# Performance work log

Hardware: AMD Instinct MI355X
Metric: run time of the kernel (lower is better)

Reference implementation:

```python
import jax, jax.numpy as jnp
import numpy as np

H = 2048  # hidden_size
B = 16    # batch
S = 2048  # source (values) length
T = 16    # decoder state length per layer
L = 1     # num_layers


def setup_inputs() -> dict:
    key = jax.random.key(0)
    ks = jax.random.split(key, 6)
    sc = 1.0 / np.sqrt(H)
    return {
        "query": jax.random.normal(ks[0], (L, B, T, H), dtype=jnp.float32),
        "values": jax.random.normal(ks[1], (B, S, H), dtype=jnp.float32),
        "mask": jnp.ones((B, S), dtype=jnp.bool_),  # unused by the module
        "W1_w": jax.random.normal(ks[2], (H, H), dtype=jnp.float32) * sc,
        "W1_b": jnp.zeros((H,), dtype=jnp.float32),
        "W2_w": jax.random.normal(ks[3], (H, H), dtype=jnp.float32) * sc,
        "W2_b": jnp.zeros((H,), dtype=jnp.float32),
        "V_w": jax.random.normal(ks[4], (H,), dtype=jnp.float32) * sc,
        "V_b": jnp.zeros((), dtype=jnp.float32),
    }


def reference(query, values, mask, W1_w, W1_b, W2_w, W2_b, V_w, V_b):
    # query: (L,B,T,H); non-bidirectional path keeps last time step of layer 0
    q = query[0][:, -1:, :]                        # (B,1,H)
    q_proj = q @ W1_w.T + W1_b                     # (B,1,H)
    # Faithful quirk of the source: W2 is applied to values[0] (batch elem 0)
    v_proj = values[0] @ W2_w.T + W2_b             # (S,H)
    # broadcast add -> (B,S,H), tanh, project with V -> (B,S)
    scores = jnp.tanh(q_proj + v_proj[None, :, :]) @ V_w + V_b  # (B,S)
    scores = scores[:, None, :]                    # (B,1,S)
    alphas = jax.nn.softmax(scores, axis=-1)       # (B,1,S)
    context = jnp.einsum('bqs,bsh->bqh', alphas, values)  # (B,1,H)
    return context, alphas
```

## Files before the change

### kernel.cpp

```cpp
#include <hip/hip_runtime.h>
#include <stdint.h>

#define H 2048
#define B 16
#define S 2048
#define SCH 32
#define SPC (S / SCH)

typedef __attribute__((ext_vector_type(4))) float f32x4;
typedef __attribute__((ext_vector_type(8))) __bf16 bf16x8;
typedef __attribute__((ext_vector_type(4))) short s16x4;

__device__ inline unsigned short f2bf(float f) {
    uint32_t u = __builtin_bit_cast(uint32_t, f);
    uint32_t r = (u + 0x7FFFu + ((u >> 16) & 1u)) >> 16;
    return (unsigned short)r;
}

__device__ inline void global_load_lds16(const unsigned short* g, unsigned short* l) {
    __builtin_amdgcn_global_load_lds(
        (const __attribute__((address_space(1))) void*)g,
        (__attribute__((address_space(3))) void*)l, 16, 0, 0);
}

__global__ __launch_bounds__(256) void convert2_kernel(
    const float* __restrict__ v0, const float* __restrict__ w2,
    unsigned short* __restrict__ Vb, unsigned short* __restrict__ W2b)
{
    const int n4 = (S * H) / 4;
    int i = blockIdx.x * blockDim.x + threadIdx.x;
    int stride = gridDim.x * blockDim.x;
    for (; i < 2 * n4; i += stride) {
        const float* src = (i < n4) ? v0 : w2;
        unsigned short* dst = (i < n4) ? Vb : W2b;
        int j = (i < n4) ? i : i - n4;
        f32x4 v = ((const f32x4*)src)[j];
        s16x4 o;
        #pragma unroll
        for (int k = 0; k < 4; ++k) o[k] = (short)f2bf(v[k]);
        ((s16x4*)dst)[j] = o;
    }
}

__global__ __launch_bounds__(256) void qproj_kernel(
    const float* __restrict__ query,
    const float* __restrict__ w1,
    const float* __restrict__ w1b,
    const float* __restrict__ w2b,
    float* __restrict__ qproj)
{
    int wid = threadIdx.x >> 6;
    int lane = threadIdx.x & 63;
    int h = blockIdx.x * 4 + wid;
    float acc[B];
    #pragma unroll
    for (int b = 0; b < B; ++b) acc[b] = 0.f;
    const float* wrow = w1 + (int64_t)h * H;
    for (int kc = 0; kc < H; kc += 256) {
        f32x4 w4 = *(const f32x4*)(wrow + kc + lane * 4);
        #pragma unroll
        for (int b = 0; b < B; ++b) {
            const float* q = query + ((int64_t)(b * 16 + 15)) * H + kc + lane * 4;
            f32x4 q4 = *(const f32x4*)q;
            acc[b] += w4.x * q4.x + w4.y * q4.y + w4.z * q4.z + w4.w * q4.w;
        }
    }
    #pragma unroll
    for (int b = 0; b < B; ++b) {
        float v = acc[b];
        #pragma unroll
        for (int off = 32; off > 0; off >>= 1) v += __shfl_down(v, off, 64);
        if (lane == 0) qproj[b * H + h] = v + w1b[h] + w2b[h];
    }
}

#define GM 64
#define GN 128
#define GK 64
#define NT (H / GK)

__global__ __launch_bounds__(256) void gemm_bt_kernel(
    const unsigned short* __restrict__ A,
    const unsigned short* __restrict__ Bm,
    float* __restrict__ C)
{
    __shared__ unsigned short smA[3][GM * GK];
    __shared__ unsigned short smB[3][GN * GK];

    int t = threadIdx.x;
    int lane = t & 63;
    int wid = t >> 6;
    int wr = wid >> 1, wc = wid & 1;
    int brow = blockIdx.y * GM;
    int bcol = blockIdx.x * GN;
    int l15 = lane & 15;

    f32x4 acc[2][4] = {};

    int srow = t >> 3;
    int kslot = (t & 7) ^ (srow & 7);
    const unsigned short* gA = A + (int64_t)(brow + srow) * H + kslot * 8;
    const unsigned short* gB = Bm + (int64_t)(bcol + srow) * H + kslot * 8;

    unsigned short* pA0 = smA[0]; unsigned short* pB0 = smB[0];
    unsigned short* pA1 = smA[1]; unsigned short* pB1 = smB[1];
    unsigned short* pA2 = smA[2]; unsigned short* pB2 = smB[2];

#define STAGE(pa, pb, koff) do {                                        \
        global_load_lds16(gA + (koff), (pa) + t * 8);                   \
        global_load_lds16(gA + 32 * H + (koff), (pa) + (t + 256) * 8);  \
        global_load_lds16(gB + (koff), (pb) + t * 8);                   \
        global_load_lds16(gB + 32 * H + (koff), (pb) + (t + 256) * 8);  \
        global_load_lds16(gB + 64 * H + (koff), (pb) + (t + 512) * 8);  \
        global_load_lds16(gB + 96 * H + (koff), (pb) + (t + 768) * 8);  \
    } while (0)

    int swz = (((lane >> 4) ^ (lane & 7)) << 3);

    STAGE(pA0, pB0, 0);
    STAGE(pA1, pB1, GK);
    asm volatile("s_waitcnt vmcnt(6)" ::: "memory");
    __builtin_amdgcn_s_barrier();
    __builtin_amdgcn_sched_barrier(0);

    for (int kt = 0; kt < NT; ++kt) {
        int kn = (kt + 2) * GK;
        if (kn < H) STAGE(pA2, pB2, kn);
        #pragma unroll
        for (int kk = 0; kk < 2; ++kk) {
            int sw = swz ^ (kk << 5);
            bf16x8 a[2], b[4];
            #pragma unroll
            for (int m = 0; m < 2; ++m)
                a[m] = *(const bf16x8*)&pA0[(wr * 32 + m * 16 + l15) * GK + sw];
            #pragma unroll
            for (int n = 0; n < 4; ++n)
                b[n] = *(const bf16x8*)&pB0[(wc * 64 + n * 16 + l15) * GK + sw];
            #pragma unroll
            for (int m = 0; m < 2; ++m)
                #pragma unroll
                for (int n = 0; n < 4; ++n)
                    acc[m][n] = __builtin_amdgcn_mfma_f32_16x16x32_bf16(a[m], b[n], acc[m][n], 0, 0, 0);
        }
        if (kn < H) asm volatile("s_waitcnt vmcnt(6)" ::: "memory");
        else        asm volatile("s_waitcnt vmcnt(0)" ::: "memory");
        __builtin_amdgcn_s_barrier();
        __builtin_amdgcn_sched_barrier(0);
        unsigned short* tmp;
        tmp = pA0; pA0 = pA1; pA1 = pA2; pA2 = tmp;
        tmp = pB0; pB0 = pB1; pB1 = pB2; pB2 = tmp;
    }
#undef STAGE

    #pragma unroll
    for (int m = 0; m < 2; ++m) {
        #pragma unroll
        for (int n = 0; n < 4; ++n) {
            int col = bcol + wc * 64 + n * 16 + l15;
            #pragma unroll
            for (int q = 0; q < 4; ++q) {
                int row = brow + wr * 32 + m * 16 + (lane >> 4) * 4 + q;
                C[(int64_t)row * H + col] = acc[m][n][q];
            }
        }
    }
}

#define K2LOG2E 2.8853900817779268f

__global__ __launch_bounds__(256) void scores_kernel(
    const float* __restrict__ vproj,
    const float* __restrict__ qproj,
    const float* __restrict__ vw,
    float* __restrict__ scores)
{
    int wid = threadIdx.x >> 6, lane = threadIdx.x & 63;
    int s = blockIdx.x * 4 + wid;
    float acc[B];
    #pragma unroll
    for (int b = 0; b < B; ++b) acc[b] = 0.f;
    const float* vrow = vproj + (int64_t)s * H;
    for (int hc = 0; hc < H; hc += 256) {
        f32x4 vp = *(const f32x4*)(vrow + hc + lane * 4);
        f32x4 w4 = *(const f32x4*)(vw + hc + lane * 4);
        #pragma unroll
        for (int b = 0; b < B; ++b) {
            f32x4 q4 = *(const f32x4*)(qproj + b * H + hc + lane * 4);
            #pragma unroll
            for (int j = 0; j < 4; ++j) {
                float x = q4[j] + vp[j];
                float e = __builtin_amdgcn_exp2f(x * K2LOG2E);
                float r = __builtin_amdgcn_rcpf(e + 1.0f);
                acc[b] = fmaf(w4[j], r, acc[b]);
            }
        }
    }
    #pragma unroll
    for (int b = 0; b < B; ++b) {
        float v = acc[b];
        #pragma unroll
        for (int off = 32; off > 0; off >>= 1) v += __shfl_down(v, off, 64);
        if (lane == 0) scores[b * S + s] = -2.0f * v;
    }
}

__global__ __launch_bounds__(256) void context_partial_kernel(
    const float* __restrict__ values,
    const float* __restrict__ scores,
    float* __restrict__ alphas,
    float* __restrict__ partial)
{
    __shared__ float red[8];
    __shared__ float a_lds[SPC];
    int ht = blockIdx.x;
    int sc = blockIdx.y;
    int b  = blockIdx.z;
    int t = threadIdx.x, wid = t >> 6, lane = t & 63;

    const float* srow = scores + b * S;
    float v[8];
    float m = -1e30f;
    #pragma unroll
    for (int i = 0; i < 8; ++i) { v[i] = srow[t + i * 256]; m = fmaxf(m, v[i]); }
    #pragma unroll
    for (int off = 32; off > 0; off >>= 1) m = fmaxf(m, __shfl_xor(m, off, 64));
    if (lane == 0) red[wid] = m;
    __syncthreads();
    m = fmaxf(fmaxf(red[0], red[1]), fmaxf(red[2], red[3]));
    float sum = 0.f;
    #pragma unroll
    for (int i = 0; i < 8; ++i) sum += __expf(v[i] - m);
    #pragma unroll
    for (int off = 32; off > 0; off >>= 1) sum += __shfl_xor(sum, off, 64);
    if (lane == 0) red[4 + wid] = sum;
    __syncthreads();
    float inv = 1.f / (red[4] + red[5] + red[6] + red[7]);

    if (t < SPC) {
        float a = __expf(srow[sc * SPC + t] - m) * inv;
        a_lds[t] = a;
        if (ht == 0) alphas[b * S + sc * SPC + t] = a;
    }
    __syncthreads();

    int h = ht * 1024 + t * 4;
    const float* vbase = values + (int64_t)b * S * H + (int64_t)sc * SPC * H + h;
    f32x4 acc0 = {}, acc1 = {};
    #pragma unroll 4
    for (int s = 0; s < SPC; s += 2) {
        float a0 = a_lds[s], a1 = a_lds[s + 1];
        f32x4 v0 = *(const f32x4*)(vbase + (int64_t)s * H);
        f32x4 v1 = *(const f32x4*)(vbase + (int64_t)(s + 1) * H);
        acc0 += a0 * v0;
        acc1 += a1 * v1;
    }
    *(f32x4*)(partial + ((int64_t)(sc * B + b)) * H + h) = acc0 + acc1;
}

__global__ __launch_bounds__(256) void context_reduce_kernel(
    const float* __restrict__ partial, float* __restrict__ out)
{
    int idx = blockIdx.x * 256 + threadIdx.x;
    int b = idx >> 11, h = idx & 2047;
    float s = 0.f;
    #pragma unroll
    for (int c = 0; c < SCH; ++c) s += partial[((int64_t)(c * B + b)) * H + h];
    out[idx] = s;
}

extern "C" void kernel_launch(void* const* d_in, const int* in_sizes, int n_in,
                              void* d_out, int out_size, void* d_ws, size_t ws_size,
                              hipStream_t stream) {
    const float* query  = (const float*)d_in[0];
    const float* values = (const float*)d_in[1];
    const float* w1w = (const float*)d_in[3];
    const float* w1b = (const float*)d_in[4];
    const float* w2w = (const float*)d_in[5];
    const float* w2b = (const float*)d_in[6];
    const float* vw  = (const float*)d_in[7];

    float* out = (float*)d_out;
    float* context = out;
    float* alphas  = out + B * H;

    float* ws = (float*)d_ws;
    float* qproj   = ws;
    float* scores  = ws + 32768;
    float* vproj   = ws + 65536;
    float* partial = vproj + (int64_t)S * H;
    unsigned short* Vb  = (unsigned short*)(partial + SCH * B * H);
    unsigned short* W2b = Vb + S * H;

    convert2_kernel<<<2048, 256, 0, stream>>>(values, w2w, Vb, W2b);
    qproj_kernel<<<H / 4, 256, 0, stream>>>(query, w1w, w1b, w2b, qproj);
    gemm_bt_kernel<<<dim3(H / GN, S / GM), 256, 0, stream>>>(Vb, W2b, vproj);
    scores_kernel<<<S / 4, 256, 0, stream>>>(vproj, qproj, vw, scores);
    context_partial_kernel<<<dim3(2, SCH, B), 256, 0, stream>>>(values, scores, alphas, partial);
    context_reduce_kernel<<<(B * H) / 256, 256, 0, stream>>>(partial, context);
}
```

Measured before the change: 133.1 us.

## Enlarge GEMM tile to 128x128 and compute two rows per wave in scores

```diff
diff --git a/kernel.cpp b/kernel.cpp
--- a/kernel.cpp
+++ b/kernel.cpp
@@ -74,8 +74,8 @@
     }
 }
 
-#define GM 64
-#define GN 128
+#define GBM 128
+#define GBN 128
 #define GK 64
 #define NT (H / GK)
 
@@ -84,18 +84,18 @@
     const unsigned short* __restrict__ Bm,
     float* __restrict__ C)
 {
-    __shared__ unsigned short smA[3][GM * GK];
-    __shared__ unsigned short smB[3][GN * GK];
+    __shared__ unsigned short smA[3][GBM * GK];
+    __shared__ unsigned short smB[3][GBN * GK];
 
     int t = threadIdx.x;
     int lane = t & 63;
     int wid = t >> 6;
     int wr = wid >> 1, wc = wid & 1;
-    int brow = blockIdx.y * GM;
-    int bcol = blockIdx.x * GN;
+    int brow = blockIdx.y * GBM;
+    int bcol = blockIdx.x * GBN;
     int l15 = lane & 15;
 
-    f32x4 acc[2][4] = {};
+    f32x4 acc[4][4] = {};
 
     int srow = t >> 3;
     int kslot = (t & 7) ^ (srow & 7);
@@ -109,6 +109,8 @@
 #define STAGE(pa, pb, koff) do {                                        \
         global_load_lds16(gA + (koff), (pa) + t * 8);                   \
         global_load_lds16(gA + 32 * H + (koff), (pa) + (t + 256) * 8);  \
+        global_load_lds16(gA + 64 * H + (koff), (pa) + (t + 512) * 8);  \
+        global_load_lds16(gA + 96 * H + (koff), (pa) + (t + 768) * 8);  \
         global_load_lds16(gB + (koff), (pb) + t * 8);                   \
         global_load_lds16(gB + 32 * H + (koff), (pb) + (t + 256) * 8);  \
         global_load_lds16(gB + 64 * H + (koff), (pb) + (t + 512) * 8);  \
@@ -119,7 +121,7 @@
 
     STAGE(pA0, pB0, 0);
     STAGE(pA1, pB1, GK);
-    asm volatile("s_waitcnt vmcnt(6)" ::: "memory");
+    asm volatile("s_waitcnt vmcnt(8)" ::: "memory");
     __builtin_amdgcn_s_barrier();
     __builtin_amdgcn_sched_barrier(0);
 
@@ -129,20 +131,20 @@
         #pragma unroll
         for (int kk = 0; kk < 2; ++kk) {
             int sw = swz ^ (kk << 5);
-            bf16x8 a[2], b[4];
-            #pragma unroll
-            for (int m = 0; m < 2; ++m)
-                a[m] = *(const bf16x8*)&pA0[(wr * 32 + m * 16 + l15) * GK + sw];
+            bf16x8 a[4], b[4];
+            #pragma unroll
+            for (int m = 0; m < 4; ++m)
+                a[m] = *(const bf16x8*)&pA0[(wr * 64 + m * 16 + l15) * GK + sw];
             #pragma unroll
             for (int n = 0; n < 4; ++n)
                 b[n] = *(const bf16x8*)&pB0[(wc * 64 + n * 16 + l15) * GK + sw];
             #pragma unroll
-            for (int m = 0; m < 2; ++m)
+            for (int m = 0; m < 4; ++m)
                 #pragma unroll
                 for (int n = 0; n < 4; ++n)
                     acc[m][n] = __builtin_amdgcn_mfma_f32_16x16x32_bf16(a[m], b[n], acc[m][n], 0, 0, 0);
         }
-        if (kn < H) asm volatile("s_waitcnt vmcnt(6)" ::: "memory");
+        if (kn < H) asm volatile("s_waitcnt vmcnt(8)" ::: "memory");
         else        asm volatile("s_waitcnt vmcnt(0)" ::: "memory");
         __builtin_amdgcn_s_barrier();
         __builtin_amdgcn_sched_barrier(0);
@@ -153,13 +155,13 @@
 #undef STAGE
 
     #pragma unroll
-    for (int m = 0; m < 2; ++m) {
+    for (int m = 0; m < 4; ++m) {
         #pragma unroll
         for (int n = 0; n < 4; ++n) {
             int col = bcol + wc * 64 + n * 16 + l15;
             #pragma unroll
             for (int q = 0; q < 4; ++q) {
-                int row = brow + wr * 32 + m * 16 + (lane >> 4) * 4 + q;
+                int row = brow + wr * 64 + m * 16 + (lane >> 4) * 4 + q;
                 C[(int64_t)row * H + col] = acc[m][n][q];
             }
         }
@@ -175,32 +177,43 @@
     float* __restrict__ scores)
 {
     int wid = threadIdx.x >> 6, lane = threadIdx.x & 63;
-    int s = blockIdx.x * 4 + wid;
-    float acc[B];
-    #pragma unroll
-    for (int b = 0; b < B; ++b) acc[b] = 0.f;
-    const float* vrow = vproj + (int64_t)s * H;
+    int s = blockIdx.x * 8 + wid * 2;
+    float acc0[B], acc1[B];
+    #pragma unroll
+    for (int b = 0; b < B; ++b) { acc0[b] = 0.f; acc1[b] = 0.f; }
+    const float* vr0 = vproj + (int64_t)s * H;
+    const float* vr1 = vr0 + H;
     for (int hc = 0; hc < H; hc += 256) {
-        f32x4 vp = *(const f32x4*)(vrow + hc + lane * 4);
-        f32x4 w4 = *(const f32x4*)(vw + hc + lane * 4);
+        int off = hc + lane * 4;
+        f32x4 vpa = *(const f32x4*)(vr0 + off);
+        f32x4 vpb = *(const f32x4*)(vr1 + off);
+        f32x4 w4  = *(const f32x4*)(vw + off);
         #pragma unroll
         for (int b = 0; b < B; ++b) {
-            f32x4 q4 = *(const f32x4*)(qproj + b * H + hc + lane * 4);
+            f32x4 q4 = *(const f32x4*)(qproj + b * H + off);
             #pragma unroll
             for (int j = 0; j < 4; ++j) {
-                float x = q4[j] + vp[j];
-                float e = __builtin_amdgcn_exp2f(x * K2LOG2E);
-                float r = __builtin_amdgcn_rcpf(e + 1.0f);
-                acc[b] = fmaf(w4[j], r, acc[b]);
+                float xa = q4[j] + vpa[j];
+                float ea = __builtin_amdgcn_exp2f(xa * K2LOG2E);
+                acc0[b] = fmaf(w4[j], __builtin_amdgcn_rcpf(ea + 1.0f), acc0[b]);
+                float xb = q4[j] + vpb[j];
+                float eb = __builtin_amdgcn_exp2f(xb * K2LOG2E);
+                acc1[b] = fmaf(w4[j], __builtin_amdgcn_rcpf(eb + 1.0f), acc1[b]);
             }
         }
     }
     #pragma unroll
     for (int b = 0; b < B; ++b) {
-        float v = acc[b];
-        #pragma unroll
-        for (int off = 32; off > 0; off >>= 1) v += __shfl_down(v, off, 64);
-        if (lane == 0) scores[b * S + s] = -2.0f * v;
+        float v0 = acc0[b], v1 = acc1[b];
+        #pragma unroll
+        for (int off = 32; off > 0; off >>= 1) {
+            v0 += __shfl_down(v0, off, 64);
+            v1 += __shfl_down(v1, off, 64);
+        }
+        if (lane == 0) {
+            scores[b * S + s]     = -2.0f * v0;
+            scores[b * S + s + 1] = -2.0f * v1;
+        }
     }
 }
 
@@ -293,8 +306,8 @@
 
     convert2_kernel<<<2048, 256, 0, stream>>>(values, w2w, Vb, W2b);
     qproj_kernel<<<H / 4, 256, 0, stream>>>(query, w1w, w1b, w2b, qproj);
-    gemm_bt_kernel<<<dim3(H / GN, S / GM), 256, 0, stream>>>(Vb, W2b, vproj);
-    scores_kernel<<<S / 4, 256, 0, stream>>>(vproj, qproj, vw, scores);
+    gemm_bt_kernel<<<dim3(H / GBN, S / GBM), 256, 0, stream>>>(Vb, W2b, vproj);
+    scores_kernel<<<S / 8, 256, 0, stream>>>(vproj, qproj, vw, scores);
     context_partial_kernel<<<dim3(2, SCH, B), 256, 0, stream>>>(values, scores, alphas, partial);
     context_reduce_kernel<<<(B * H) / 256, 256, 0, stream>>>(partial, context);
 }
```

New measurement: 175.7 us. 32.0% more time.
